# Kernel optimization log

Measured on AMD Instinct MI355X. Metric: run time of the kernel, lower is better.

## Reference

```python
import jax, jax.numpy as jnp
import numpy as np

D_MODEL = 768
NUM_HEADS = 12
D_K = D_MODEL // NUM_HEADS  # 64


def setup_inputs() -> dict:
    key = jax.random.key(0)
    ks = jax.random.split(key, 7)
    B, S = 2, 4096
    Q = jax.random.normal(ks[0], (B, S, D_MODEL), dtype=jnp.float32)
    K = jax.random.normal(ks[1], (B, S, D_MODEL), dtype=jnp.float32)
    V = jax.random.normal(ks[2], (B, S, D_MODEL), dtype=jnp.float32)
    scale = 1.0 / np.sqrt(D_MODEL)
    # Per-head projection weights stacked: [H, d_model, d_k] (equivalent to
    # the torch per-head nn.Linear(d_model, d_k, bias=False) applied as x @ W)
    WQ = jax.random.normal(ks[3], (NUM_HEADS, D_MODEL, D_K), dtype=jnp.float32) * scale
    WK = jax.random.normal(ks[4], (NUM_HEADS, D_MODEL, D_K), dtype=jnp.float32) * scale
    WV = jax.random.normal(ks[5], (NUM_HEADS, D_MODEL, D_K), dtype=jnp.float32) * scale
    # Output projection: [num_head*d_v, d_model]
    WO = jax.random.normal(ks[6], (NUM_HEADS * D_K, D_MODEL), dtype=jnp.float32) * scale
    return {"Q": Q, "K": K, "V": V, "WQ": WQ, "WK": WK, "WV": WV, "WO": WO}


def reference(Q, K, V, WQ, WK, WV, WO):
    # Per-head projections (batched over heads): [B,H,S,d_k]
    q = jnp.einsum('bsd,hdk->bhsk', Q, WQ)
    k = jnp.einsum('bsd,hdk->bhsk', K, WK)
    v = jnp.einsum('bsd,hdk->bhsk', V, WV)
    # Full attention scores: [B,H,S,S]
    scores = jnp.einsum('bhqd,bhsd->bhqs', q, k) / jnp.sqrt(jnp.asarray(D_K, q.dtype))
    attn = jax.nn.softmax(scores, axis=-1)  # dropout_p=0 -> identity
    out = jnp.einsum('bhqs,bhsd->bhqd', attn, v)  # [B,H,S,d_k]
    # Concatenate heads along feature dim (head order = concat order)
    B, H, S, Dk = out.shape
    out = out.transpose(0, 2, 1, 3).reshape(B, S, H * Dk)
    return out @ WO  # [B,S,d_model]
```

## Files before the change

### kernel.cpp

```cpp
#include <hip/hip_runtime.h>
#include <hip/hip_bf16.h>
#include <stdint.h>
#include <stddef.h>

#define NH 12
#define DKH 64
#define DM 768
#define SS 4096

typedef __attribute__((ext_vector_type(8))) short bf16x8;
typedef __attribute__((ext_vector_type(4))) float f32x4;
typedef __attribute__((ext_vector_type(16))) float f32x16;

__device__ __forceinline__ unsigned short f2bf(float x) {
  union { float f; unsigned int u; } a; a.f = x;
  unsigned int r = a.u + 0x7fffu + ((a.u >> 16) & 1u);
  return (unsigned short)(r >> 16);
}

__device__ __forceinline__ unsigned pkbf2(float a, float b) {
  union { __hip_bfloat162 h; unsigned u; } x;
  x.h = __float22bfloat162_rn(float2{a, b});
  return x.u;
}

__device__ __forceinline__ unsigned cvt_pk_bf16(float lo, float hi) {
  unsigned r;
  asm("v_cvt_pk_bf16_f32 %0, %1, %2" : "=v"(r) : "v"(lo), "v"(hi));
  return r;
}

__device__ __forceinline__ void plane32_swap(unsigned& a, unsigned& b) {
  asm("v_permlane32_swap_b32 %0, %1" : "+v"(a), "+v"(b));
}

__device__ __forceinline__ float fast_exp2(float x) {
#if __has_builtin(__builtin_amdgcn_exp2f)
  return __builtin_amdgcn_exp2f(x);
#else
  return exp2f(x);
#endif
}

__device__ __forceinline__ void gload16(const void* g, void* l) {
  __builtin_amdgcn_global_load_lds(
      (const __attribute__((address_space(1))) void*)g,
      (__attribute__((address_space(3))) void*)l, 16, 0, 0);
}

__global__ __launch_bounds__(256) void conv_weights(
    const float* __restrict__ WQ, const float* __restrict__ WK,
    const float* __restrict__ WV, const float* __restrict__ WO,
    unsigned short* __restrict__ wq, unsigned short* __restrict__ wk,
    unsigned short* __restrict__ wv, unsigned short* __restrict__ wo) {
  int idx = blockIdx.x * 256 + threadIdx.x;
  if (idx >= DM * DM) return;
  int n = idx / DM, k = idx % DM;
  int src = ((n >> 6) * DM + k) * DKH + (n & 63);
  wq[idx] = f2bf(WQ[src] * 0.18033688011112042f);
  wk[idx] = f2bf(WK[src]);
  wv[idx] = f2bf(WV[src]);
  wo[idx] = f2bf(WO[k * DM + n]);
}

__global__ __launch_bounds__(256) void proj_gemm3(
    const float* __restrict__ Qin, const float* __restrict__ Kin,
    const float* __restrict__ Vin, const unsigned short* __restrict__ Wbase,
    unsigned short* __restrict__ Obase) {
  __shared__ unsigned short Bs[128 * 64];
  __shared__ unsigned short As[128 * 72];
  const int z = blockIdx.z;
  const float* A = (z == 0) ? Qin : (z == 1) ? Kin : Vin;
  const unsigned short* Wt = Wbase + (size_t)z * DM * DM;
  unsigned short* out = Obase + (size_t)z * 2 * NH * SS * DKH;

  const int tid = threadIdx.x;
  const int lane = tid & 63, wave = tid >> 6;
  const int wm = wave >> 1, wn = wave & 1;
  const int l15 = lane & 15, lhi = lane >> 4;
  const int m0 = blockIdx.y * 128, n0 = blockIdx.x * 128;
  const int lrow = lane >> 3, lchunk = lane & 7;
  const int schunk = lchunk ^ lrow;
  const int arow = tid >> 1, ahalf = tid & 1;

  f32x4 acc[4][4] = {};

  for (int k0 = 0; k0 < DM; k0 += 64) {
#pragma unroll
    for (int i = 0; i < 4; ++i) {
      int r = wave * 32 + i * 8;
      gload16(Wt + (size_t)(n0 + r + lrow) * DM + k0 + schunk * 8, &Bs[r * 64]);
    }
    {
      const float* ap = A + (size_t)(m0 + arow) * DM + k0 + ahalf * 32;
      float4 f0 = *(const float4*)(ap + 0);
      float4 f1 = *(const float4*)(ap + 4);
      float4 f2 = *(const float4*)(ap + 8);
      float4 f3 = *(const float4*)(ap + 12);
      float4 f4 = *(const float4*)(ap + 16);
      float4 f5 = *(const float4*)(ap + 20);
      float4 f6 = *(const float4*)(ap + 24);
      float4 f7 = *(const float4*)(ap + 28);
      union { unsigned u[4]; uint4 v; } p0, p1, p2, p3;
      p0.u[0] = pkbf2(f0.x, f0.y); p0.u[1] = pkbf2(f0.z, f0.w);
      p0.u[2] = pkbf2(f1.x, f1.y); p0.u[3] = pkbf2(f1.z, f1.w);
      p1.u[0] = pkbf2(f2.x, f2.y); p1.u[1] = pkbf2(f2.z, f2.w);
      p1.u[2] = pkbf2(f3.x, f3.y); p1.u[3] = pkbf2(f3.z, f3.w);
      p2.u[0] = pkbf2(f4.x, f4.y); p2.u[1] = pkbf2(f4.z, f4.w);
      p2.u[2] = pkbf2(f5.x, f5.y); p2.u[3] = pkbf2(f5.z, f5.w);
      p3.u[0] = pkbf2(f6.x, f6.y); p3.u[1] = pkbf2(f6.z, f6.w);
      p3.u[2] = pkbf2(f7.x, f7.y); p3.u[3] = pkbf2(f7.z, f7.w);
      unsigned short* as = &As[arow * 72 + ahalf * 32];
      *(uint4*)(as + 0) = p0.v;
      *(uint4*)(as + 8) = p1.v;
      *(uint4*)(as + 16) = p2.v;
      *(uint4*)(as + 24) = p3.v;
    }
    __syncthreads();

    bf16x8 af[4][2], bfr[4][2];
#pragma unroll
    for (int m = 0; m < 4; ++m) {
      int row = wm * 64 + m * 16 + l15;
#pragma unroll
      for (int ks = 0; ks < 2; ++ks)
        af[m][ks] = *(const bf16x8*)&As[row * 72 + ks * 32 + lhi * 8];
    }
#pragma unroll
    for (int n = 0; n < 4; ++n) {
      int row = wn * 64 + n * 16 + l15;
#pragma unroll
      for (int ks = 0; ks < 2; ++ks)
        bfr[n][ks] = *(const bf16x8*)&Bs[row * 64 + (((ks * 4 + lhi) ^ (row & 7)) * 8)];
    }
#pragma unroll
    for (int ks = 0; ks < 2; ++ks)
#pragma unroll
      for (int m = 0; m < 4; ++m)
#pragma unroll
        for (int n = 0; n < 4; ++n)
          acc[m][n] = __builtin_amdgcn_mfma_f32_16x16x32_bf16(af[m][ks], bfr[n][ks], acc[m][n], 0, 0, 0);
    __syncthreads();
  }

#pragma unroll
  for (int m = 0; m < 4; ++m) {
#pragma unroll
    for (int r = 0; r < 4; ++r) {
      int row = m0 + wm * 64 + m * 16 + lhi * 4 + r;
      int b = row >> 12, s = row & 4095;
#pragma unroll
      for (int n = 0; n < 4; ++n) {
        int col = n0 + wn * 64 + n * 16 + l15;
        int h = col >> 6, dk = col & 63;
        size_t dst;
        if (z == 2) dst = ((size_t)(b * NH + h) * DKH + dk) * SS + s;
        else        dst = ((size_t)(b * NH + h) * SS + s) * DKH + dk;
        out[dst] = f2bf(acc[m][n][r]);
      }
    }
  }
}

__device__ __forceinline__ void pack_pb(const f32x16& s0, const f32x16& s1, bf16x8* pb) {
#pragma unroll
  for (int h2 = 0; h2 < 2; ++h2) {
    unsigned c0a = cvt_pk_bf16(s0[8 * h2 + 0], s0[8 * h2 + 1]);
    unsigned c1a = cvt_pk_bf16(s0[8 * h2 + 2], s0[8 * h2 + 3]);
    unsigned c0b = cvt_pk_bf16(s0[8 * h2 + 4], s0[8 * h2 + 5]);
    unsigned c1b = cvt_pk_bf16(s0[8 * h2 + 6], s0[8 * h2 + 7]);
    plane32_swap(c0a, c0b);
    plane32_swap(c1a, c1b);
    union { unsigned u[4]; bf16x8 v; } f;
    f.u[0] = c0a; f.u[1] = c1a; f.u[2] = c0b; f.u[3] = c1b;
    pb[h2] = f.v;
  }
#pragma unroll
  for (int h2 = 0; h2 < 2; ++h2) {
    unsigned c0a = cvt_pk_bf16(s1[8 * h2 + 0], s1[8 * h2 + 1]);
    unsigned c1a = cvt_pk_bf16(s1[8 * h2 + 2], s1[8 * h2 + 3]);
    unsigned c0b = cvt_pk_bf16(s1[8 * h2 + 4], s1[8 * h2 + 5]);
    unsigned c1b = cvt_pk_bf16(s1[8 * h2 + 6], s1[8 * h2 + 7]);
    plane32_swap(c0a, c0b);
    plane32_swap(c1a, c1b);
    union { unsigned u[4]; bf16x8 v; } f;
    f.u[0] = c0a; f.u[1] = c1a; f.u[2] = c0b; f.u[3] = c1b;
    pb[2 + h2] = f.v;
  }
}

__device__ __forceinline__ float tree16(const f32x16& v) {
  float a = (v[0] + v[1]) + (v[2] + v[3]);
  float b = (v[4] + v[5]) + (v[6] + v[7]);
  float c = (v[8] + v[9]) + (v[10] + v[11]);
  float d = (v[12] + v[13]) + (v[14] + v[15]);
  return (a + b) + (c + d);
}

__global__ __launch_bounds__(256, 2) void flash_attn(
    const unsigned short* __restrict__ Qp, const unsigned short* __restrict__ Kp,
    const unsigned short* __restrict__ Vt, unsigned short* __restrict__ Ao) {
  __shared__ unsigned short LDSu[2][2][8192];
  float* Ob = (float*)&LDSu[0][0][0];
  float* Lb = (float*)&LDSu[1][0][0];
  const int tid = threadIdx.x;
  const int lane = tid & 63, wave = tid >> 6;
  const int pair = wave >> 1, wp = wave & 1;
  const int ql = lane & 31, hi = lane >> 5;
  const int bh = blockIdx.y, b = bh / NH, h = bh % NH;
  const int q0 = blockIdx.x * 128 + wp * 64;
  const int kvbase = pair * (SS / 2);

  bf16x8 qf0[4], qf1[4];
  {
    const unsigned short* qb = Qp + ((size_t)bh * SS + q0 + ql) * DKH;
#pragma unroll
    for (int s = 0; s < 4; ++s) {
      qf0[s] = *(const bf16x8*)(qb + s * 16 + hi * 8);
      qf1[s] = *(const bf16x8*)(qb + 32 * DKH + s * 16 + hi * 8);
    }
  }

  const unsigned short* gK = Kp + (size_t)bh * SS * DKH;
  const unsigned short* gV = Vt + (size_t)bh * DKH * SS;
  const int lrow = lane >> 3;
  const int sch = ((lane & 7) ^ lrow) * 8;
  const int xs = (ql & 7) << 3;

  unsigned short* KV0 = &LDSu[pair][0][0];
  unsigned short* KV1 = &LDSu[pair][1][0];

#pragma unroll
  for (int i = 0; i < 4; ++i) {
    int r = wp * 32 + i * 8;
    gload16(gK + (size_t)(kvbase + r + lrow) * DKH + sch, KV0 + r * 64);
    gload16(gV + (size_t)(r + lrow) * SS + kvbase + sch, KV0 + 4096 + r * 64);
  }

  f32x16 oA = {}, oB = {}, oC = {}, oD = {};
  float lp0 = 0.f, lp1 = 0.f;

  for (int it = 0; it < 32; ++it) {
    asm volatile("s_waitcnt vmcnt(0)" ::: "memory");
    __builtin_amdgcn_s_barrier();
    __builtin_amdgcn_sched_barrier(0);
    unsigned short* cur = (it & 1) ? KV1 : KV0;
    unsigned short* nxt = (it & 1) ? KV0 : KV1;
    if (it + 1 < 32) {
      int kvn = kvbase + (it + 1) * 64;
#pragma unroll
      for (int i = 0; i < 4; ++i) {
        int r = wp * 32 + i * 8;
        gload16(gK + (size_t)(kvn + r + lrow) * DKH + sch, nxt + r * 64);
        gload16(gV + (size_t)(r + lrow) * SS + kvn + sch, nxt + 4096 + r * 64);
      }
    }
    const unsigned short* Ks = cur;
    const unsigned short* Vs = cur + 4096;

    f32x16 s00 = {}, s01 = {}, s10 = {}, s11 = {};
    __builtin_amdgcn_s_setprio(1);
#pragma unroll
    for (int s = 0; s < 4; ++s) {
      bf16x8 ka0 = *(const bf16x8*)&Ks[ql * 64 + ((s * 16 + hi * 8) ^ xs)];
      bf16x8 ka1 = *(const bf16x8*)&Ks[(32 + ql) * 64 + ((s * 16 + hi * 8) ^ xs)];
      s00 = __builtin_amdgcn_mfma_f32_32x32x16_bf16(ka0, qf0[s], s00, 0, 0, 0);
      s10 = __builtin_amdgcn_mfma_f32_32x32x16_bf16(ka0, qf1[s], s10, 0, 0, 0);
      s01 = __builtin_amdgcn_mfma_f32_32x32x16_bf16(ka1, qf0[s], s01, 0, 0, 0);
      s11 = __builtin_amdgcn_mfma_f32_32x32x16_bf16(ka1, qf1[s], s11, 0, 0, 0);
    }
    __builtin_amdgcn_s_setprio(0);

#pragma unroll
    for (int r = 0; r < 16; ++r) s00[r] = fast_exp2(s00[r]);
#pragma unroll
    for (int r = 0; r < 16; ++r) s01[r] = fast_exp2(s01[r]);
#pragma unroll
    for (int r = 0; r < 16; ++r) s10[r] = fast_exp2(s10[r]);
#pragma unroll
    for (int r = 0; r < 16; ++r) s11[r] = fast_exp2(s11[r]);
    lp0 += tree16(s00) + tree16(s01);
    lp1 += tree16(s10) + tree16(s11);

    bf16x8 pb0[4], pb1[4];
    pack_pb(s00, s01, pb0);
    pack_pb(s10, s11, pb1);

    __builtin_amdgcn_s_setprio(1);
#pragma unroll
    for (int ks = 0; ks < 4; ++ks) {
      bf16x8 va0 = *(const bf16x8*)&Vs[ql * 64 + ((ks * 16 + hi * 8) ^ xs)];
      bf16x8 va1 = *(const bf16x8*)&Vs[(32 + ql) * 64 + ((ks * 16 + hi * 8) ^ xs)];
      oA = __builtin_amdgcn_mfma_f32_32x32x16_bf16(va0, pb0[ks], oA, 0, 0, 0);
      oB = __builtin_amdgcn_mfma_f32_32x32x16_bf16(va1, pb0[ks], oB, 0, 0, 0);
      oC = __builtin_amdgcn_mfma_f32_32x32x16_bf16(va0, pb1[ks], oC, 0, 0, 0);
      oD = __builtin_amdgcn_mfma_f32_32x32x16_bf16(va1, pb1[ks], oD, 0, 0, 0);
    }
    __builtin_amdgcn_s_setprio(0);
  }

  float l0 = lp0 + __shfl_xor(lp0, 32);
  float l1 = lp1 + __shfl_xor(lp1, 32);
  const int qq0 = wp * 64 + ql, qq1 = wp * 64 + 32 + ql;
  const int swz0 = (qq0 & 7) << 3, swz1 = (qq1 & 7) << 3;

  __syncthreads();
  if (pair == 0) {
#pragma unroll
    for (int g = 0; g < 4; ++g) {
      int d0 = hi * 4 + g * 8;
      *(float4*)&Ob[qq0 * 64 + (d0 ^ swz0)] = float4{oA[4 * g], oA[4 * g + 1], oA[4 * g + 2], oA[4 * g + 3]};
      *(float4*)&Ob[qq0 * 64 + ((d0 + 32) ^ swz0)] = float4{oB[4 * g], oB[4 * g + 1], oB[4 * g + 2], oB[4 * g + 3]};
      *(float4*)&Ob[qq1 * 64 + (d0 ^ swz1)] = float4{oC[4 * g], oC[4 * g + 1], oC[4 * g + 2], oC[4 * g + 3]};
      *(float4*)&Ob[qq1 * 64 + ((d0 + 32) ^ swz1)] = float4{oD[4 * g], oD[4 * g + 1], oD[4 * g + 2], oD[4 * g + 3]};
    }
    if (hi == 0) { Lb[qq0] = l0; Lb[qq1] = l1; }
  }
  __syncthreads();
  if (pair == 1) {
    float inv0 = 1.0f / (l0 + Lb[qq0]);
    float inv1 = 1.0f / (l1 + Lb[qq1]);
#pragma unroll
    for (int g = 0; g < 4; ++g) {
      int d0 = hi * 4 + g * 8;
      float4 pA = *(const float4*)&Ob[qq0 * 64 + (d0 ^ swz0)];
      float4 pB = *(const float4*)&Ob[qq0 * 64 + ((d0 + 32) ^ swz0)];
      float4 pC = *(const float4*)&Ob[qq1 * 64 + (d0 ^ swz1)];
      float4 pD = *(const float4*)&Ob[qq1 * 64 + ((d0 + 32) ^ swz1)];
      oA[4 * g] += pA.x; oA[4 * g + 1] += pA.y; oA[4 * g + 2] += pA.z; oA[4 * g + 3] += pA.w;
      oB[4 * g] += pB.x; oB[4 * g + 1] += pB.y; oB[4 * g + 2] += pB.z; oB[4 * g + 3] += pB.w;
      oC[4 * g] += pC.x; oC[4 * g + 1] += pC.y; oC[4 * g + 2] += pC.z; oC[4 * g + 3] += pC.w;
      oD[4 * g] += pD.x; oD[4 * g + 1] += pD.y; oD[4 * g + 2] += pD.z; oD[4 * g + 3] += pD.w;
    }
    unsigned short* orow0 = Ao + ((size_t)b * SS + q0 + ql) * DM + h * DKH;
    unsigned short* orow1 = Ao + ((size_t)b * SS + q0 + 32 + ql) * DM + h * DKH;
#pragma unroll
    for (int g = 0; g < 4; ++g) {
      int d0 = g * 8 + hi * 4;
      *(unsigned*)&orow0[d0]          = cvt_pk_bf16(oA[4 * g + 0] * inv0, oA[4 * g + 1] * inv0);
      *(unsigned*)&orow0[d0 + 2]      = cvt_pk_bf16(oA[4 * g + 2] * inv0, oA[4 * g + 3] * inv0);
      *(unsigned*)&orow0[32 + d0]     = cvt_pk_bf16(oB[4 * g + 0] * inv0, oB[4 * g + 1] * inv0);
      *(unsigned*)&orow0[32 + d0 + 2] = cvt_pk_bf16(oB[4 * g + 2] * inv0, oB[4 * g + 3] * inv0);
      *(unsigned*)&orow1[d0]          = cvt_pk_bf16(oC[4 * g + 0] * inv1, oC[4 * g + 1] * inv1);
      *(unsigned*)&orow1[d0 + 2]      = cvt_pk_bf16(oC[4 * g + 2] * inv1, oC[4 * g + 3] * inv1);
      *(unsigned*)&orow1[32 + d0]     = cvt_pk_bf16(oD[4 * g + 0] * inv1, oD[4 * g + 1] * inv1);
      *(unsigned*)&orow1[32 + d0 + 2] = cvt_pk_bf16(oD[4 * g + 2] * inv1, oD[4 * g + 3] * inv1);
    }
  }
}

__global__ __launch_bounds__(256) void out_gemm(
    const unsigned short* __restrict__ A, const unsigned short* __restrict__ Wt,
    float* __restrict__ out) {
  __shared__ unsigned short Bs[128 * 64];
  __shared__ unsigned short As[64 * 64];
  const int tid = threadIdx.x;
  const int lane = tid & 63, wave = tid >> 6;
  const int wm = wave >> 1, wn = wave & 1;
  const int l15 = lane & 15, lhi = lane >> 4;
  const int m0 = blockIdx.y * 64, n0 = blockIdx.x * 128;
  const int lrow = lane >> 3;
  const int schunk = (lane & 7) ^ lrow;

  f32x4 acc[2][4] = {};

  for (int k0 = 0; k0 < DM; k0 += 64) {
#pragma unroll
    for (int i = 0; i < 4; ++i) {
      int r = wave * 32 + i * 8;
      gload16(Wt + (size_t)(n0 + r + lrow) * DM + k0 + schunk * 8, &Bs[r * 64]);
    }
#pragma unroll
    for (int i = 0; i < 2; ++i) {
      int r = wave * 16 + i * 8;
      gload16(A + (size_t)(m0 + r + lrow) * DM + k0 + schunk * 8, &As[r * 64]);
    }
    __syncthreads();

    bf16x8 af[2][2], bfr[4][2];
#pragma unroll
    for (int m = 0; m < 2; ++m) {
      int row = wm * 32 + m * 16 + l15;
#pragma unroll
      for (int ks = 0; ks < 2; ++ks)
        af[m][ks] = *(const bf16x8*)&As[row * 64 + (((ks * 4 + lhi) ^ (row & 7)) * 8)];
    }
#pragma unroll
    for (int n = 0; n < 4; ++n) {
      int row = wn * 64 + n * 16 + l15;
#pragma unroll
      for (int ks = 0; ks < 2; ++ks)
        bfr[n][ks] = *(const bf16x8*)&Bs[row * 64 + (((ks * 4 + lhi) ^ (row & 7)) * 8)];
    }
#pragma unroll
    for (int ks = 0; ks < 2; ++ks)
#pragma unroll
      for (int m = 0; m < 2; ++m)
#pragma unroll
        for (int n = 0; n < 4; ++n)
          acc[m][n] = __builtin_amdgcn_mfma_f32_16x16x32_bf16(af[m][ks], bfr[n][ks], acc[m][n], 0, 0, 0);
    __syncthreads();
  }

#pragma unroll
  for (int m = 0; m < 2; ++m)
#pragma unroll
    for (int r = 0; r < 4; ++r) {
      int row = m0 + wm * 32 + m * 16 + lhi * 4 + r;
#pragma unroll
      for (int n = 0; n < 4; ++n) {
        int col = n0 + wn * 64 + n * 16 + l15;
        out[(size_t)row * DM + col] = acc[m][n][r];
      }
    }
}

extern "C" void kernel_launch(void* const* d_in, const int* in_sizes, int n_in,
                              void* d_out, int out_size, void* d_ws, size_t ws_size,
                              hipStream_t stream) {
  const float* Q  = (const float*)d_in[0];
  const float* K  = (const float*)d_in[1];
  const float* V  = (const float*)d_in[2];
  const float* WQ = (const float*)d_in[3];
  const float* WK = (const float*)d_in[4];
  const float* WV = (const float*)d_in[5];
  const float* WO = (const float*)d_in[6];
  char* ws = (char*)d_ws;

  const size_t WSZ = (size_t)DM * DM * 2;
  const size_t PSZ = (size_t)2 * NH * SS * DKH * 2;
  unsigned short* w_base = (unsigned short*)(ws);
  unsigned short* wo_t   = (unsigned short*)(ws + 3 * WSZ);
  unsigned short* p_base = (unsigned short*)(ws + 4 * WSZ);
  unsigned short* q_p  = (unsigned short*)(ws + 4 * WSZ);
  unsigned short* k_p  = (unsigned short*)(ws + 4 * WSZ + PSZ);
  unsigned short* v_t  = (unsigned short*)(ws + 4 * WSZ + 2 * PSZ);
  unsigned short* attn = (unsigned short*)(ws + 4 * WSZ + 3 * PSZ);

  conv_weights<<<(DM * DM + 255) / 256, 256, 0, stream>>>(
      WQ, WK, WV, WO, w_base, w_base + WSZ / 2, w_base + WSZ, wo_t);

  proj_gemm3<<<dim3(DM / 128, (2 * SS) / 128, 3), 256, 0, stream>>>(Q, K, V, w_base, p_base);

  flash_attn<<<dim3(SS / 128, 2 * NH), 256, 0, stream>>>(q_p, k_p, v_t, attn);

  out_gemm<<<dim3(DM / 128, (2 * SS) / 64), 256, 0, stream>>>(attn, wo_t, d_out ? (float*)d_out : nullptr);
}
```

Measured before the change: 255.1 us.

## Pre-convert QKV to bf16, double-buffer GEMMs, split K/V staging in attention

A separate kernel now converts the fp32 Q/K/V inputs to bf16, so the projection GEMM can stage both operands with async global-to-LDS loads. The projection GEMM uses 128x96 tiles with double buffering and remapped block order, and it swaps MFMA operands for V so the transposed store coalesces. Flash attention gets separate K double buffers and a single V buffer with finer waits, so it fits three blocks per CU. The output GEMM is also double-buffered with a remapped grid. The costs are an extra pass over the inputs through memory and more workspace.

```diff
diff --git a/kernel.cpp b/kernel.cpp
--- a/kernel.cpp
+++ b/kernel.cpp
@@ -63,100 +63,130 @@
   wo[idx] = f2bf(WO[k * DM + n]);
 }
 
-__global__ __launch_bounds__(256) void proj_gemm3(
-    const float* __restrict__ Qin, const float* __restrict__ Kin,
-    const float* __restrict__ Vin, const unsigned short* __restrict__ Wbase,
+__global__ __launch_bounds__(256) void qkv_conv(
+    const float* __restrict__ Q, const float* __restrict__ K,
+    const float* __restrict__ V, unsigned short* __restrict__ out) {
+  int gid = blockIdx.x * 256 + threadIdx.x;
+  int t = gid / 786432, e = gid % 786432;
+  const float* src = (t == 0) ? Q : (t == 1) ? K : V;
+  float4 a = *(const float4*)(src + (size_t)e * 8);
+  float4 c = *(const float4*)(src + (size_t)e * 8 + 4);
+  union { unsigned u[4]; uint4 v; } o;
+  o.u[0] = pkbf2(a.x, a.y); o.u[1] = pkbf2(a.z, a.w);
+  o.u[2] = pkbf2(c.x, c.y); o.u[3] = pkbf2(c.z, c.w);
+  *(uint4*)(out + (size_t)t * 6291456 + (size_t)e * 8) = o.v;
+}
+
+__global__ __launch_bounds__(256, 2) void proj_gemm3(
+    const unsigned short* __restrict__ Abase,
+    const unsigned short* __restrict__ Wbase,
     unsigned short* __restrict__ Obase) {
-  __shared__ unsigned short Bs[128 * 64];
-  __shared__ unsigned short As[128 * 72];
-  const int z = blockIdx.z;
-  const float* A = (z == 0) ? Qin : (z == 1) ? Kin : Vin;
-  const unsigned short* Wt = Wbase + (size_t)z * DM * DM;
-  unsigned short* out = Obase + (size_t)z * 2 * NH * SS * DKH;
-
+  __shared__ unsigned short As[2][128 * 64];
+  __shared__ unsigned short Bs[2][96 * 64];
   const int tid = threadIdx.x;
   const int lane = tid & 63, wave = tid >> 6;
   const int wm = wave >> 1, wn = wave & 1;
   const int l15 = lane & 15, lhi = lane >> 4;
-  const int m0 = blockIdx.y * 128, n0 = blockIdx.x * 128;
-  const int lrow = lane >> 3, lchunk = lane & 7;
-  const int schunk = lchunk ^ lrow;
-  const int arow = tid >> 1, ahalf = tid & 1;
-
-  f32x4 acc[4][4] = {};
-
-  for (int k0 = 0; k0 < DM; k0 += 64) {
+  const int lrow = lane >> 3;
+  const int schunk = (lane & 7) ^ lrow;
+
+  int fid = blockIdx.x + (blockIdx.y << 3) + (blockIdx.z << 9);
+  int nid = (fid & 7) * 192 + (fid >> 3);
+  const int bx = nid & 7;
+  const int rem = nid >> 3;
+  const int by = rem & 63, z = rem >> 6;
+  const bool z2 = (z == 2);
+
+  const unsigned short* A = Abase + (size_t)z * 6291456;
+  const unsigned short* Wt = Wbase + (size_t)z * DM * DM;
+  unsigned short* out = Obase + (size_t)z * 2 * NH * SS * DKH;
+  const int m0 = by * 128, n0 = bx * 96;
+
+  auto stage = [&](int k0, int buf) {
 #pragma unroll
     for (int i = 0; i < 4; ++i) {
       int r = wave * 32 + i * 8;
-      gload16(Wt + (size_t)(n0 + r + lrow) * DM + k0 + schunk * 8, &Bs[r * 64]);
-    }
-    {
-      const float* ap = A + (size_t)(m0 + arow) * DM + k0 + ahalf * 32;
-      float4 f0 = *(const float4*)(ap + 0);
-      float4 f1 = *(const float4*)(ap + 4);
-      float4 f2 = *(const float4*)(ap + 8);
-      float4 f3 = *(const float4*)(ap + 12);
-      float4 f4 = *(const float4*)(ap + 16);
-      float4 f5 = *(const float4*)(ap + 20);
-      float4 f6 = *(const float4*)(ap + 24);
-      float4 f7 = *(const float4*)(ap + 28);
-      union { unsigned u[4]; uint4 v; } p0, p1, p2, p3;
-      p0.u[0] = pkbf2(f0.x, f0.y); p0.u[1] = pkbf2(f0.z, f0.w);
-      p0.u[2] = pkbf2(f1.x, f1.y); p0.u[3] = pkbf2(f1.z, f1.w);
-      p1.u[0] = pkbf2(f2.x, f2.y); p1.u[1] = pkbf2(f2.z, f2.w);
-      p1.u[2] = pkbf2(f3.x, f3.y); p1.u[3] = pkbf2(f3.z, f3.w);
-      p2.u[0] = pkbf2(f4.x, f4.y); p2.u[1] = pkbf2(f4.z, f4.w);
-      p2.u[2] = pkbf2(f5.x, f5.y); p2.u[3] = pkbf2(f5.z, f5.w);
-      p3.u[0] = pkbf2(f6.x, f6.y); p3.u[1] = pkbf2(f6.z, f6.w);
-      p3.u[2] = pkbf2(f7.x, f7.y); p3.u[3] = pkbf2(f7.z, f7.w);
-      unsigned short* as = &As[arow * 72 + ahalf * 32];
-      *(uint4*)(as + 0) = p0.v;
-      *(uint4*)(as + 8) = p1.v;
-      *(uint4*)(as + 16) = p2.v;
-      *(uint4*)(as + 24) = p3.v;
-    }
-    __syncthreads();
-
-    bf16x8 af[4][2], bfr[4][2];
+      gload16(A + (size_t)(m0 + r + lrow) * DM + k0 + schunk * 8, &As[buf][r * 64]);
+    }
+#pragma unroll
+    for (int i = 0; i < 3; ++i) {
+      int r = wave * 24 + i * 8;
+      gload16(Wt + (size_t)(n0 + r + lrow) * DM + k0 + schunk * 8, &Bs[buf][r * 64]);
+    }
+  };
+
+  f32x4 acc[4][3] = {};
+
+  stage(0, 0);
+  stage(64, 1);
+
+  for (int t = 0; t < 12; ++t) {
+    asm volatile("s_waitcnt vmcnt(7)" ::: "memory");
+    asm volatile("s_barrier" ::: "memory");
+    const int buf = t & 1;
+    bf16x8 af[4][2], bfr[3][2];
 #pragma unroll
     for (int m = 0; m < 4; ++m) {
       int row = wm * 64 + m * 16 + l15;
 #pragma unroll
       for (int ks = 0; ks < 2; ++ks)
-        af[m][ks] = *(const bf16x8*)&As[row * 72 + ks * 32 + lhi * 8];
-    }
-#pragma unroll
-    for (int n = 0; n < 4; ++n) {
-      int row = wn * 64 + n * 16 + l15;
+        af[m][ks] = *(const bf16x8*)&As[buf][row * 64 + (((ks * 4 + lhi) ^ (row & 7)) * 8)];
+    }
+#pragma unroll
+    for (int n = 0; n < 3; ++n) {
+      int row = wn * 48 + n * 16 + l15;
 #pragma unroll
       for (int ks = 0; ks < 2; ++ks)
-        bfr[n][ks] = *(const bf16x8*)&Bs[row * 64 + (((ks * 4 + lhi) ^ (row & 7)) * 8)];
-    }
+        bfr[n][ks] = *(const bf16x8*)&Bs[buf][row * 64 + (((ks * 4 + lhi) ^ (row & 7)) * 8)];
+    }
+    asm volatile("s_waitcnt lgkmcnt(0)" ::: "memory");
+    asm volatile("s_barrier" ::: "memory");
+    int kt = (t + 2 < 12) ? (t + 2) * 64 : 0;
+    stage(kt, buf);
+    __builtin_amdgcn_s_setprio(1);
 #pragma unroll
     for (int ks = 0; ks < 2; ++ks)
 #pragma unroll
       for (int m = 0; m < 4; ++m)
 #pragma unroll
-        for (int n = 0; n < 4; ++n)
-          acc[m][n] = __builtin_amdgcn_mfma_f32_16x16x32_bf16(af[m][ks], bfr[n][ks], acc[m][n], 0, 0, 0);
-    __syncthreads();
-  }
-
-#pragma unroll
-  for (int m = 0; m < 4; ++m) {
-#pragma unroll
-    for (int r = 0; r < 4; ++r) {
-      int row = m0 + wm * 64 + m * 16 + lhi * 4 + r;
-      int b = row >> 12, s = row & 4095;
-#pragma unroll
-      for (int n = 0; n < 4; ++n) {
-        int col = n0 + wn * 64 + n * 16 + l15;
-        int h = col >> 6, dk = col & 63;
-        size_t dst;
-        if (z == 2) dst = ((size_t)(b * NH + h) * DKH + dk) * SS + s;
-        else        dst = ((size_t)(b * NH + h) * SS + s) * DKH + dk;
-        out[dst] = f2bf(acc[m][n][r]);
+        for (int n = 0; n < 3; ++n) {
+          if (z2)
+            acc[m][n] = __builtin_amdgcn_mfma_f32_16x16x32_bf16(bfr[n][ks], af[m][ks], acc[m][n], 0, 0, 0);
+          else
+            acc[m][n] = __builtin_amdgcn_mfma_f32_16x16x32_bf16(af[m][ks], bfr[n][ks], acc[m][n], 0, 0, 0);
+        }
+    __builtin_amdgcn_s_setprio(0);
+  }
+  asm volatile("s_waitcnt vmcnt(0)" ::: "memory");
+
+  if (!z2) {
+#pragma unroll
+    for (int m = 0; m < 4; ++m) {
+#pragma unroll
+      for (int r = 0; r < 4; ++r) {
+        int row = m0 + wm * 64 + m * 16 + lhi * 4 + r;
+        int bb = row >> 12, s = row & 4095;
+#pragma unroll
+        for (int n = 0; n < 3; ++n) {
+          int col = n0 + wn * 48 + n * 16 + l15;
+          int hh = col >> 6, dk = col & 63;
+          out[((size_t)(bb * NH + hh) * SS + s) * DKH + dk] = f2bf(acc[m][n][r]);
+        }
+      }
+    }
+  } else {
+#pragma unroll
+    for (int m = 0; m < 4; ++m) {
+      int srow = m0 + wm * 64 + m * 16 + l15;
+      int bb = srow >> 12, s = srow & 4095;
+#pragma unroll
+      for (int n = 0; n < 3; ++n) {
+#pragma unroll
+        for (int r = 0; r < 4; ++r) {
+          int col = n0 + wn * 48 + n * 16 + lhi * 4 + r;
+          int hh = col >> 6, dk = col & 63;
+          out[((size_t)(bb * NH + hh) * DKH + dk) * SS + s] = f2bf(acc[m][n][r]);
+        }
       }
     }
   }
@@ -197,18 +227,21 @@
   return (a + b) + (c + d);
 }
 
-__global__ __launch_bounds__(256, 2) void flash_attn(
+__global__ __launch_bounds__(256, 3) void flash_attn(
     const unsigned short* __restrict__ Qp, const unsigned short* __restrict__ Kp,
     const unsigned short* __restrict__ Vt, unsigned short* __restrict__ Ao) {
-  __shared__ unsigned short LDSu[2][2][8192];
-  float* Ob = (float*)&LDSu[0][0][0];
-  float* Lb = (float*)&LDSu[1][0][0];
+  __shared__ uint4 smem4[3120];
+  unsigned short* smem = (unsigned short*)smem4;
   const int tid = threadIdx.x;
   const int lane = tid & 63, wave = tid >> 6;
   const int pair = wave >> 1, wp = wave & 1;
   const int ql = lane & 31, hi = lane >> 5;
-  const int bh = blockIdx.y, b = bh / NH, h = bh % NH;
-  const int q0 = blockIdx.x * 128 + wp * 64;
+
+  int fid = blockIdx.x + (blockIdx.y << 5);
+  int nid = (fid & 7) * 96 + (fid >> 3);
+  const int bx = nid & 31, bh = nid >> 5;
+  const int b = bh / NH, h = bh % NH;
+  const int q0 = bx * 128 + wp * 64;
   const int kvbase = pair * (SS / 2);
 
   bf16x8 qf0[4], qf1[4];
@@ -227,36 +260,45 @@
   const int sch = ((lane & 7) ^ lrow) * 8;
   const int xs = (ql & 7) << 3;
 
-  unsigned short* KV0 = &LDSu[pair][0][0];
-  unsigned short* KV1 = &LDSu[pair][1][0];
-
-#pragma unroll
-  for (int i = 0; i < 4; ++i) {
-    int r = wp * 32 + i * 8;
-    gload16(gK + (size_t)(kvbase + r + lrow) * DKH + sch, KV0 + r * 64);
-    gload16(gV + (size_t)(r + lrow) * SS + kvbase + sch, KV0 + 4096 + r * 64);
-  }
+  unsigned short* KbA = smem + pair * 12288;
+  unsigned short* KbB = KbA + 4096;
+  unsigned short* Vb = KbA + 8192;
+  float* Ob = (float*)smem;
+  float* Lb = (float*)((char*)smem + 49152);
+
+  auto stageK = [&](int kv0, unsigned short* dst) {
+#pragma unroll
+    for (int i = 0; i < 4; ++i) {
+      int r = wp * 32 + i * 8;
+      gload16(gK + (size_t)(kv0 + r + lrow) * DKH + sch, dst + r * 64);
+    }
+  };
+  auto stageV = [&](int kv0, unsigned short* dst) {
+#pragma unroll
+    for (int i = 0; i < 4; ++i) {
+      int r = wp * 32 + i * 8;
+      gload16(gV + (size_t)(r + lrow) * SS + kv0 + sch, dst + r * 64);
+    }
+  };
+
+  stageK(kvbase, KbA);
+  stageV(kvbase, Vb);
 
   f32x16 oA = {}, oB = {}, oC = {}, oD = {};
   float lp0 = 0.f, lp1 = 0.f;
 
   for (int it = 0; it < 32; ++it) {
-    asm volatile("s_waitcnt vmcnt(0)" ::: "memory");
-    __builtin_amdgcn_s_barrier();
+    const unsigned short* Ks = (it & 1) ? KbB : KbA;
+    unsigned short* Kn = (it & 1) ? KbA : KbB;
+    const bool notlast = (it < 31);
+    if (notlast) {
+      stageK(kvbase + (it + 1) * 64, Kn);
+      asm volatile("s_waitcnt vmcnt(8)" ::: "memory");
+    } else {
+      asm volatile("s_waitcnt vmcnt(4)" ::: "memory");
+    }
+    asm volatile("s_barrier" ::: "memory");
     __builtin_amdgcn_sched_barrier(0);
-    unsigned short* cur = (it & 1) ? KV1 : KV0;
-    unsigned short* nxt = (it & 1) ? KV0 : KV1;
-    if (it + 1 < 32) {
-      int kvn = kvbase + (it + 1) * 64;
-#pragma unroll
-      for (int i = 0; i < 4; ++i) {
-        int r = wp * 32 + i * 8;
-        gload16(gK + (size_t)(kvn + r + lrow) * DKH + sch, nxt + r * 64);
-        gload16(gV + (size_t)(r + lrow) * SS + kvn + sch, nxt + 4096 + r * 64);
-      }
-    }
-    const unsigned short* Ks = cur;
-    const unsigned short* Vs = cur + 4096;
 
     f32x16 s00 = {}, s01 = {}, s10 = {}, s11 = {};
     __builtin_amdgcn_s_setprio(1);
@@ -286,17 +328,25 @@
     pack_pb(s00, s01, pb0);
     pack_pb(s10, s11, pb1);
 
+    if (notlast) asm volatile("s_waitcnt vmcnt(4)" ::: "memory");
+    else         asm volatile("s_waitcnt vmcnt(0)" ::: "memory");
+    asm volatile("s_barrier" ::: "memory");
+
     __builtin_amdgcn_s_setprio(1);
 #pragma unroll
     for (int ks = 0; ks < 4; ++ks) {
-      bf16x8 va0 = *(const bf16x8*)&Vs[ql * 64 + ((ks * 16 + hi * 8) ^ xs)];
-      bf16x8 va1 = *(const bf16x8*)&Vs[(32 + ql) * 64 + ((ks * 16 + hi * 8) ^ xs)];
+      bf16x8 va0 = *(const bf16x8*)&Vb[ql * 64 + ((ks * 16 + hi * 8) ^ xs)];
+      bf16x8 va1 = *(const bf16x8*)&Vb[(32 + ql) * 64 + ((ks * 16 + hi * 8) ^ xs)];
       oA = __builtin_amdgcn_mfma_f32_32x32x16_bf16(va0, pb0[ks], oA, 0, 0, 0);
       oB = __builtin_amdgcn_mfma_f32_32x32x16_bf16(va1, pb0[ks], oB, 0, 0, 0);
       oC = __builtin_amdgcn_mfma_f32_32x32x16_bf16(va0, pb1[ks], oC, 0, 0, 0);
       oD = __builtin_amdgcn_mfma_f32_32x32x16_bf16(va1, pb1[ks], oD, 0, 0, 0);
     }
     __builtin_amdgcn_s_setprio(0);
+
+    asm volatile("s_waitcnt lgkmcnt(0)" ::: "memory");
+    asm volatile("s_barrier" ::: "memory");
+    if (notlast) stageV(kvbase + (it + 1) * 64, Vb);
   }
 
   float l0 = lp0 + __shfl_xor(lp0, 32);
@@ -349,49 +399,64 @@
   }
 }
 
-__global__ __launch_bounds__(256) void out_gemm(
+__global__ __launch_bounds__(256, 3) void out_gemm(
     const unsigned short* __restrict__ A, const unsigned short* __restrict__ Wt,
     float* __restrict__ out) {
-  __shared__ unsigned short Bs[128 * 64];
-  __shared__ unsigned short As[64 * 64];
+  __shared__ unsigned short As[2][64 * 64];
+  __shared__ unsigned short Bs[2][128 * 64];
   const int tid = threadIdx.x;
   const int lane = tid & 63, wave = tid >> 6;
   const int wm = wave >> 1, wn = wave & 1;
   const int l15 = lane & 15, lhi = lane >> 4;
-  const int m0 = blockIdx.y * 64, n0 = blockIdx.x * 128;
   const int lrow = lane >> 3;
   const int schunk = (lane & 7) ^ lrow;
 
-  f32x4 acc[2][4] = {};
-
-  for (int k0 = 0; k0 < DM; k0 += 64) {
+  int fid = blockIdx.x + 6 * blockIdx.y;
+  int nid = (fid & 7) * 96 + (fid >> 3);
+  const int bx = nid % 6, by = nid / 6;
+  const int m0 = by * 64, n0 = bx * 128;
+
+  auto stage = [&](int k0, int buf) {
 #pragma unroll
     for (int i = 0; i < 4; ++i) {
       int r = wave * 32 + i * 8;
-      gload16(Wt + (size_t)(n0 + r + lrow) * DM + k0 + schunk * 8, &Bs[r * 64]);
+      gload16(Wt + (size_t)(n0 + r + lrow) * DM + k0 + schunk * 8, &Bs[buf][r * 64]);
     }
 #pragma unroll
     for (int i = 0; i < 2; ++i) {
       int r = wave * 16 + i * 8;
-      gload16(A + (size_t)(m0 + r + lrow) * DM + k0 + schunk * 8, &As[r * 64]);
-    }
-    __syncthreads();
-
+      gload16(A + (size_t)(m0 + r + lrow) * DM + k0 + schunk * 8, &As[buf][r * 64]);
+    }
+  };
+
+  f32x4 acc[2][4] = {};
+  stage(0, 0);
+  stage(64, 1);
+
+  for (int t = 0; t < 12; ++t) {
+    asm volatile("s_waitcnt vmcnt(6)" ::: "memory");
+    asm volatile("s_barrier" ::: "memory");
+    const int buf = t & 1;
     bf16x8 af[2][2], bfr[4][2];
 #pragma unroll
     for (int m = 0; m < 2; ++m) {
       int row = wm * 32 + m * 16 + l15;
 #pragma unroll
       for (int ks = 0; ks < 2; ++ks)
-        af[m][ks] = *(const bf16x8*)&As[row * 64 + (((ks * 4 + lhi) ^ (row & 7)) * 8)];
+        af[m][ks] = *(const bf16x8*)&As[buf][row * 64 + (((ks * 4 + lhi) ^ (row & 7)) * 8)];
     }
 #pragma unroll
     for (int n = 0; n < 4; ++n) {
       int row = wn * 64 + n * 16 + l15;
 #pragma unroll
       for (int ks = 0; ks < 2; ++ks)
-        bfr[n][ks] = *(const bf16x8*)&Bs[row * 64 + (((ks * 4 + lhi) ^ (row & 7)) * 8)];
-    }
+        bfr[n][ks] = *(const bf16x8*)&Bs[buf][row * 64 + (((ks * 4 + lhi) ^ (row & 7)) * 8)];
+    }
+    asm volatile("s_waitcnt lgkmcnt(0)" ::: "memory");
+    asm volatile("s_barrier" ::: "memory");
+    int kt = (t + 2 < 12) ? (t + 2) * 64 : 0;
+    stage(kt, buf);
+    __builtin_amdgcn_s_setprio(1);
 #pragma unroll
     for (int ks = 0; ks < 2; ++ks)
 #pragma unroll
@@ -399,8 +464,9 @@
 #pragma unroll
         for (int n = 0; n < 4; ++n)
           acc[m][n] = __builtin_amdgcn_mfma_f32_16x16x32_bf16(af[m][ks], bfr[n][ks], acc[m][n], 0, 0, 0);
-    __syncthreads();
-  }
+    __builtin_amdgcn_s_setprio(0);
+  }
+  asm volatile("s_waitcnt vmcnt(0)" ::: "memory");
 
 #pragma unroll
   for (int m = 0; m < 2; ++m)
@@ -428,21 +494,24 @@
   char* ws = (char*)d_ws;
 
   const size_t WSZ = (size_t)DM * DM * 2;
-  const size_t PSZ = (size_t)2 * NH * SS * DKH * 2;
-  unsigned short* w_base = (unsigned short*)(ws);
-  unsigned short* wo_t   = (unsigned short*)(ws + 3 * WSZ);
-  unsigned short* p_base = (unsigned short*)(ws + 4 * WSZ);
-  unsigned short* q_p  = (unsigned short*)(ws + 4 * WSZ);
-  unsigned short* k_p  = (unsigned short*)(ws + 4 * WSZ + PSZ);
-  unsigned short* v_t  = (unsigned short*)(ws + 4 * WSZ + 2 * PSZ);
-  unsigned short* attn = (unsigned short*)(ws + 4 * WSZ + 3 * PSZ);
+  const size_t ABF = (size_t)2 * SS * DM * 2;
+  unsigned short* w_base  = (unsigned short*)(ws);
+  unsigned short* wo_t    = (unsigned short*)(ws + 3 * WSZ);
+  unsigned short* qkv_bf  = (unsigned short*)(ws + 4 * WSZ);
+  unsigned short* p_base  = (unsigned short*)(ws + 4 * WSZ + 3 * ABF);
+  unsigned short* q_p  = p_base;
+  unsigned short* k_p  = p_base + ABF / 2;
+  unsigned short* v_t  = p_base + ABF;
+  unsigned short* attn = p_base + 3 * (ABF / 2);
 
   conv_weights<<<(DM * DM + 255) / 256, 256, 0, stream>>>(
       WQ, WK, WV, WO, w_base, w_base + WSZ / 2, w_base + WSZ, wo_t);
 
-  proj_gemm3<<<dim3(DM / 128, (2 * SS) / 128, 3), 256, 0, stream>>>(Q, K, V, w_base, p_base);
+  qkv_conv<<<9216, 256, 0, stream>>>(Q, K, V, qkv_bf);
+
+  proj_gemm3<<<dim3(8, 64, 3), 256, 0, stream>>>(qkv_bf, w_base, p_base);
 
   flash_attn<<<dim3(SS / 128, 2 * NH), 256, 0, stream>>>(q_p, k_p, v_t, attn);
 
-  out_gemm<<<dim3(DM / 128, (2 * SS) / 64), 256, 0, stream>>>(attn, wo_t, d_out ? (float*)d_out : nullptr);
-}
+  out_gemm<<<dim3(6, 128), 256, 0, stream>>>(attn, wo_t, (float*)d_out);
+}
```

New measurement: 686.2 us. 2.69x slower.
